# Kernel tuning notes

Measured on AMD Instinct MI355X. Metric: run time of the kernel, lower is better.

Reference implementation:

```python
import jax, jax.numpy as jnp
import numpy as np

N_NODES = 10000
N_EDGES = 640000
F_IN = 128
HID = 128
F_OUT = 40
BN_EPS = 1e-5


def setup_inputs() -> dict:
    key = jax.random.key(0)
    ks = jax.random.split(key, 8)
    x = jax.random.normal(ks[0], (N_NODES, F_IN), dtype=jnp.float32)
    edge_row = jax.random.randint(ks[1], (N_EDGES,), 0, N_NODES)
    edge_col = jax.random.randint(ks[2], (N_EDGES,), 0, N_NODES)
    edge_val = jax.random.uniform(ks[3], (N_EDGES,), dtype=jnp.float32)
    W1 = jax.random.normal(ks[4], (F_IN, HID), dtype=jnp.float32) * 0.05
    W2 = jax.random.normal(ks[5], (HID, HID), dtype=jnp.float32) * 0.05
    W3 = jax.random.normal(ks[6], (HID, F_OUT), dtype=jnp.float32) * 0.05
    return {
        "x": x, "edge_row": edge_row, "edge_col": edge_col, "edge_val": edge_val,
        "W1": W1, "b1": jnp.zeros((HID,), jnp.float32),
        "gamma2": jnp.ones((HID,), jnp.float32), "beta2": jnp.zeros((HID,), jnp.float32),
        "W2": W2, "b2": jnp.zeros((HID,), jnp.float32),
        "gamma3": jnp.ones((HID,), jnp.float32), "beta3": jnp.zeros((HID,), jnp.float32),
        "W3": W3, "b3": jnp.zeros((F_OUT,), jnp.float32),
    }


def _spmm(edge_row, edge_col, edge_val, x, n_nodes):
    # out[i] = sum_{e: row[e]==i} val[e] * x[col[e]]  == torch.sparse.mm(adj, x)
    msgs = edge_val[:, None] * jnp.take(x, edge_col, axis=0)  # [E, F]
    return jax.ops.segment_sum(msgs, edge_row, num_segments=n_nodes)


def _batchnorm(x, gamma, beta):
    # BatchNorm1d (training-mode normalization, biased variance)
    mean = jnp.mean(x, axis=0)
    var = jnp.mean(jnp.square(x - mean), axis=0)
    return gamma * (x - mean) * jax.lax.rsqrt(var + BN_EPS) + beta


def reference(x, edge_row, edge_col, edge_val, W1, b1, gamma2, beta2,
              W2, b2, gamma3, beta3, W3, b3):
    n = x.shape[0]
    # layer 1: SpMM -> Linear -> ReLU -> (dropout=identity in eval) -> BN
    h = _spmm(edge_row, edge_col, edge_val, x, n)
    h = jax.nn.relu(h @ W1 + b1)
    h = _batchnorm(h, gamma2, beta2)
    # layer 2
    h = _spmm(edge_row, edge_col, edge_val, h, n)
    h = jax.nn.relu(h @ W2 + b2)
    h = _batchnorm(h, gamma3, beta3)
    # layer 3
    h = _spmm(edge_row, edge_col, edge_val, h, n)
    h = h @ W3 + b3
    return jax.nn.log_softmax(h, axis=1)
```

## Files before the change

kernel.cpp:

```cpp
#include <hip/hip_runtime.h>
#include <hip/hip_bf16.h>
#include <math.h>

#define N_NODES 10000
#define F 128
#define F_OUT_ 40
#define N_EDGES_ 640000
#define BN_EPS 1e-5f
#define NBIN 625
#define RPB 16
#define NWGA 256
#define EPW 2500
#define BINCAP 1536
#define NREP 8

__device__ __forceinline__ unsigned pack4(int col, float v) {
    __hip_bfloat16 b = __float2bfloat16(v);
    return ((unsigned)(*(unsigned short*)&b) << 16) | (unsigned)col;
}
__device__ __forceinline__ int   col_of(unsigned q) { return (int)(q & 0xFFFFu); }
__device__ __forceinline__ float val_of(unsigned q) { return __uint_as_float(q & 0xFFFF0000u); }
__device__ __forceinline__ float lo16f(unsigned w) { return __uint_as_float(w << 16); }
__device__ __forceinline__ float hi16f(unsigned w) { return __uint_as_float(w & 0xffff0000u); }

__global__ __launch_bounds__(256) void fused_g1h(const float* __restrict__ x,
        const float* __restrict__ W1, __hip_bfloat16* __restrict__ T,
        const int* __restrict__ erow, int* __restrict__ hist,
        float* __restrict__ accsZ ) {
    __shared__ float Ws[F * F];
    __shared__ float As[16][F];
    __shared__ int   lh[NBIN];
    int tid = threadIdx.x;
    if (blockIdx.x == 0) {
        for (int i = tid; i < 2 * NREP * 256; i += 256) accsZ[i] = 0.f;
    }
    if (blockIdx.x >= NBIN) {
        int w = blockIdx.x - NBIN;
        for (int t = tid; t < NBIN; t += 256) lh[t] = 0;
        __syncthreads();
        int e0 = w * EPW;
        for (int e = e0 + tid; e < e0 + EPW; e += 256)
            atomicAdd(&lh[erow[e] >> 4], 1);
        __syncthreads();
        for (int t = tid; t < NBIN; t += 256) hist[w * NBIN + t] = lh[t];
        return;
    }
    for (int i = tid; i < F * F; i += 256) Ws[i] = W1[i];
    int r0 = blockIdx.x * 16;
    for (int i = tid; i < 16 * F; i += 256) {
        int r2 = i >> 7, k = i & (F - 1);
        As[r2][k] = x[(size_t)(r0 + r2) * F + k];
    }
    __syncthreads();
    int c = tid & (F - 1), hh = tid >> 7;
    for (int r2 = hh; r2 < 16; r2 += 2) {
        float acc = 0.f;
        #pragma unroll
        for (int k = 0; k < F; ++k) acc = fmaf(As[r2][k], Ws[k * F + c], acc);
        T[(size_t)(r0 + r2) * F + c] = __float2bfloat16(acc);
    }
}

__global__ __launch_bounds__(1024) void scatter_bin(const int* __restrict__ erow,
                                                    const int* __restrict__ ecol,
                                                    const float* __restrict__ eval_,
                                                    const int* __restrict__ hist,
                                                    int* __restrict__ base_g,
                                                    int2* __restrict__ ebin) {
    __shared__ int myoff[NBIN];
    __shared__ int tot[NBIN];
    __shared__ int cur[NBIN];
    __shared__ int sc[1024];
    int w = blockIdx.x, tid = threadIdx.x;
    for (int b = tid; b < NBIN; b += 1024) {
        int own = 0, all = 0;
        #pragma unroll 8
        for (int w2 = 0; w2 < NWGA; ++w2) {
            int h = hist[w2 * NBIN + b];
            all += h;
            if (w2 < w) own += h;
        }
        myoff[b] = own;
        tot[b] = all;
        cur[b] = 0;
    }
    __syncthreads();
    int val = (tid < NBIN) ? tot[tid] : 0;
    sc[tid] = val;
    __syncthreads();
    for (int off = 1; off < 1024; off <<= 1) {
        int v = 0;
        if (tid >= off) v = sc[tid - off];
        __syncthreads();
        if (tid >= off) sc[tid] += v;
        __syncthreads();
    }
    if (tid < NBIN) {
        int base = sc[tid] - val;
        myoff[tid] += base;
        if (w == 0) base_g[tid] = base;
    }
    if (w == 0 && tid == 0) base_g[NBIN] = N_EDGES_;
    __syncthreads();
    int e0 = w * EPW, e1 = e0 + EPW;
    for (int e = e0 + tid; e < e1; e += 1024) {
        int r = erow[e];
        int b = r >> 4;
        int p = atomicAdd(&cur[b], 1);
        ebin[myoff[b] + p] = make_int2((r << 14) | ecol[e], __float_as_int(eval_[e]));
    }
}

__global__ __launch_bounds__(256) void sort_bin(const int* __restrict__ base,
                                                const int2* __restrict__ ebin,
                                                unsigned* __restrict__ ebin2,
                                                int* __restrict__ rowptr) {
    __shared__ int2    ein[BINCAP];
    __shared__ unsigned eout[BINCAP];
    __shared__ int cnt16[16], pos16[16], exc[16];
    int b = blockIdx.x, tid = threadIdx.x;
    int lo = base[b], hi = base[b + 1];
    int n = min(hi - lo, BINCAP);
    for (int i = tid; i < n; i += 256) ein[i] = ebin[lo + i];
    if (tid < 16) cnt16[tid] = 0;
    __syncthreads();
    for (int i = tid; i < n; i += 256)
        atomicAdd(&cnt16[(ein[i].x >> 14) & 15], 1);
    __syncthreads();
    if (tid == 0) {
        int run = 0;
        #pragma unroll
        for (int j = 0; j < 16; ++j) { exc[j] = run; run += cnt16[j]; }
    }
    __syncthreads();
    if (tid < 16) {
        pos16[tid] = exc[tid];
        rowptr[b * RPB + tid] = lo + exc[tid];
    }
    if (b == NBIN - 1 && tid == 0) rowptr[N_NODES] = hi;
    __syncthreads();
    for (int i = tid; i < n; i += 256) {
        int2 q = ein[i];
        int j = (q.x >> 14) & 15;
        int p = atomicAdd(&pos16[j], 1);
        eout[p] = pack4(q.x & 16383, __int_as_float(q.y));
    }
    __syncthreads();
    for (int i = tid; i < n; i += 256) ebin2[lo + i] = eout[i];
}

__global__ __launch_bounds__(256) void spmm_row4s(const int* __restrict__ rowptr,
                                                  const unsigned* __restrict__ epk,
                                                  const unsigned long long* __restrict__ T8,
                                                  float* __restrict__ Z,
                                                  const float* __restrict__ bias,
                                                  float* __restrict__ accs) {
    __shared__ float sacc[2][F];
    int tid = threadIdx.x;
    for (int i = tid; i < 2 * F; i += 256) ((float*)sacc)[i] = 0.f;
    __syncthreads();
    int wv = tid >> 6, lane = tid & 63;
    int r = blockIdx.x * 4 + wv;
    int beg = rowptr[r], end = rowptr[r + 1];
    int half = lane >> 5, l2 = lane & 31;
    float a0c0 = 0.f, a0c1 = 0.f, a1c0 = 0.f, a1c1 = 0.f;
    float a2c0 = 0.f, a2c1 = 0.f, a3c0 = 0.f, a3c1 = 0.f;
    for (int bb = beg; bb < end; bb += 64) {
        int m = min(end - bb, 64);
        unsigned myq = (lane < m) ? epk[bb + lane] : 0u;
        int j = 0;
        for (; j + 16 <= m; j += 16) {
            unsigned q[8]; unsigned long long w[8];
            #pragma unroll
            for (int t = 0; t < 8; ++t) {
                q[t] = __shfl(myq, j + 2 * t + half);
                w[t] = __builtin_nontemporal_load(T8 + (unsigned)col_of(q[t]) * 32u + l2);
            }
            #pragma unroll
            for (int t = 0; t < 8; ++t) {
                float v = val_of(q[t]);
                unsigned wx = (unsigned)w[t], wy = (unsigned)(w[t] >> 32);
                if (t & 1) {
                    a0c1 = fmaf(v, lo16f(wx), a0c1);
                    a1c1 = fmaf(v, hi16f(wx), a1c1);
                    a2c1 = fmaf(v, lo16f(wy), a2c1);
                    a3c1 = fmaf(v, hi16f(wy), a3c1);
                } else {
                    a0c0 = fmaf(v, lo16f(wx), a0c0);
                    a1c0 = fmaf(v, hi16f(wx), a1c0);
                    a2c0 = fmaf(v, lo16f(wy), a2c0);
                    a3c0 = fmaf(v, hi16f(wy), a3c0);
                }
            }
        }
        for (; j + 2 <= m; j += 2) {
            unsigned q = __shfl(myq, j + half);
            unsigned long long w = __builtin_nontemporal_load(T8 + (unsigned)col_of(q) * 32u + l2);
            float v = val_of(q);
            unsigned wx = (unsigned)w, wy = (unsigned)(w >> 32);
            a0c0 = fmaf(v, lo16f(wx), a0c0);
            a1c0 = fmaf(v, hi16f(wx), a1c0);
            a2c0 = fmaf(v, lo16f(wy), a2c0);
            a3c0 = fmaf(v, hi16f(wy), a3c0);
        }
        if (j < m) {
            unsigned q = __shfl(myq, j);
            unsigned long long w = __builtin_nontemporal_load(T8 + (unsigned)col_of(q) * 32u + l2);
            float v = half ? 0.f : val_of(q);
            unsigned wx = (unsigned)w, wy = (unsigned)(w >> 32);
            a0c0 = fmaf(v, lo16f(wx), a0c0);
            a1c0 = fmaf(v, hi16f(wx), a1c0);
            a2c0 = fmaf(v, lo16f(wy), a2c0);
            a3c0 = fmaf(v, hi16f(wy), a3c0);
        }
    }
    float a0 = a0c0 + a0c1, a1 = a1c0 + a1c1;
    float a2 = a2c0 + a2c1, a3 = a3c0 + a3c1;
    a0 += __shfl_xor(a0, 32);
    a1 += __shfl_xor(a1, 32);
    a2 += __shfl_xor(a2, 32);
    a3 += __shfl_xor(a3, 32);
    if (half == 0) {
        *(float4*)(Z + (size_t)r * F + 4 * l2) = make_float4(a0, a1, a2, a3);
        float4 bi = *(const float4*)(bias + 4 * l2);
        float t0 = fmaxf(a0 + bi.x, 0.f), t1 = fmaxf(a1 + bi.y, 0.f);
        float t2 = fmaxf(a2 + bi.z, 0.f), t3 = fmaxf(a3 + bi.w, 0.f);
        atomicAdd(&sacc[0][4 * l2],     t0); atomicAdd(&sacc[1][4 * l2],     t0 * t0);
        atomicAdd(&sacc[0][4 * l2 + 1], t1); atomicAdd(&sacc[1][4 * l2 + 1], t1 * t1);
        atomicAdd(&sacc[0][4 * l2 + 2], t2); atomicAdd(&sacc[1][4 * l2 + 2], t2 * t2);
        atomicAdd(&sacc[0][4 * l2 + 3], t3); atomicAdd(&sacc[1][4 * l2 + 3], t3 * t3);
    }
    __syncthreads();
    int rep = blockIdx.x & (NREP - 1);
    float* dst = accs + rep * 2 * F;
    for (int i = tid; i < F; i += 256) {
        atomicAdd(&dst[i],     sacc[0][i]);
        atomicAdd(&dst[F + i], sacc[1][i]);
    }
}

__global__ __launch_bounds__(256) void spmm40_ls(const int* __restrict__ rowptr,
                                                 const unsigned* __restrict__ epk,
                                                 const unsigned short* __restrict__ T40,
                                                 const float* __restrict__ b3,
                                                 float* __restrict__ out) {
    int wv = threadIdx.x >> 6, lane = threadIdx.x & 63;
    int w = blockIdx.x * 4 + wv;
    if (w >= N_NODES) return;
    int beg = rowptr[w], end = rowptr[w + 1];
    float a[4] = {0.f, 0.f, 0.f, 0.f};
    const unsigned short* Tb = T40 + lane;
    bool act = (lane < F_OUT_);
    for (int base = beg; base < end; base += 64) {
        int m = min(end - base, 64);
        unsigned myq = 0;
        if (lane < m) myq = epk[base + lane];
        int j = 0;
        for (; j + 8 <= m; j += 8) {
            unsigned q[8];
            #pragma unroll
            for (int t = 0; t < 8; ++t) q[t] = __shfl(myq, j + t);
            if (act) {
                unsigned short u[8];
                #pragma unroll
                for (int t = 0; t < 8; ++t)
                    u[t] = __builtin_nontemporal_load(Tb + (unsigned)col_of(q[t]) * 40u);
                #pragma unroll
                for (int t = 0; t < 8; ++t)
                    a[t & 3] = fmaf(val_of(q[t]),
                                    __uint_as_float(((unsigned)u[t]) << 16), a[t & 3]);
            }
        }
        for (; j < m; ++j) {
            unsigned q = __shfl(myq, j);
            if (act) {
                unsigned short u = __builtin_nontemporal_load(Tb + (unsigned)col_of(q) * 40u);
                a[0] = fmaf(val_of(q), __uint_as_float(((unsigned)u) << 16), a[0]);
            }
        }
    }
    float acc = (a[0] + a[1]) + (a[2] + a[3]);
    float val = act ? acc + b3[lane] : -INFINITY;
    float m2 = val;
    #pragma unroll
    for (int off = 32; off > 0; off >>= 1) m2 = fmaxf(m2, __shfl_xor(m2, off));
    float e = act ? expf(val - m2) : 0.f;
    float s = e;
    #pragma unroll
    for (int off = 32; off > 0; off >>= 1) s += __shfl_xor(s, off);
    if (act) out[(size_t)w * F_OUT_ + lane] = val - m2 - logf(s);
}


__global__ __launch_bounds__(256) void gemm128_bn(const float* __restrict__ A,
        const float* __restrict__ W, const float* __restrict__ bias,
        const float* __restrict__ gamma, const float* __restrict__ beta,
        const float* __restrict__ accs, __hip_bfloat16* __restrict__ C) {
    __shared__ float Ws[F * F];
    __shared__ float As[16][F];
    __shared__ float sc[F], sh[F], bi[F];
    int tid = threadIdx.x;
    if (tid < F) {
        float s = 0.f, s2 = 0.f;
        #pragma unroll
        for (int rp = 0; rp < NREP; ++rp) {
            s  += accs[rp * 2 * F + tid];
            s2 += accs[rp * 2 * F + F + tid];
        }
        float m   = s / (float)N_NODES;
        float var = s2 / (float)N_NODES - m * m;
        float rs  = rsqrtf(var + BN_EPS);
        float g   = gamma[tid] * rs;
        sc[tid] = g;
        sh[tid] = beta[tid] - g * m;
        bi[tid] = bias[tid];
    }
    for (int i = tid; i < F * F; i += 256) Ws[i] = W[i];
    __syncthreads();
    int r0 = blockIdx.x * 16;
    for (int i = tid; i < 16 * F; i += 256) {
        int r2 = i >> 7, k = i & (F - 1);
        float a = A[(size_t)(r0 + r2) * F + k];
        As[r2][k] = fmaxf(a + bi[k], 0.f) * sc[k] + sh[k];
    }
    __syncthreads();
    int c = tid & (F - 1), hh = tid >> 7;
    for (int r2 = hh; r2 < 16; r2 += 2) {
        float acc = 0.f;
        #pragma unroll
        for (int k = 0; k < F; ++k) acc = fmaf(As[r2][k], Ws[k * F + c], acc);
        C[(size_t)(r0 + r2) * F + c] = __float2bfloat16(acc);
    }
}

__global__ __launch_bounds__(256) void gemm40_bn(const float* __restrict__ A,
        const float* __restrict__ W, const float* __restrict__ bias,
        const float* __restrict__ gamma, const float* __restrict__ beta,
        const float* __restrict__ accs, __hip_bfloat16* __restrict__ C) {
    __shared__ float Ws[F * F_OUT_];
    __shared__ float sc[F], sh[F], bi[F];
    int tid = threadIdx.x;
    if (tid < F) {
        float s = 0.f, s2 = 0.f;
        #pragma unroll
        for (int rp = 0; rp < NREP; ++rp) {
            s  += accs[rp * 2 * F + tid];
            s2 += accs[rp * 2 * F + F + tid];
        }
        float m   = s / (float)N_NODES;
        float var = s2 / (float)N_NODES - m * m;
        float rs  = rsqrtf(var + BN_EPS);
        float g   = gamma[tid] * rs;
        sc[tid] = g;
        sh[tid] = beta[tid] - g * m;
        bi[tid] = bias[tid];
    }
    for (int i = tid; i < F * F_OUT_; i += 256) Ws[i] = W[i];
    __syncthreads();
    int c = tid % F_OUT_, rl = tid / F_OUT_;
    if (rl >= 6) return;
    int r = blockIdx.x * 6 + rl;
    if (r >= N_NODES) return;
    const float* a = A + (size_t)r * F;
    float acc = 0.f;
    #pragma unroll
    for (int k = 0; k < F; ++k) {
        float t = fmaxf(a[k] + bi[k], 0.f) * sc[k] + sh[k];
        acc = fmaf(t, Ws[k * F_OUT_ + c], acc);
    }
    C[(size_t)r * F_OUT_ + c] = __float2bfloat16(acc);
}


extern "C" void kernel_launch(void* const* d_in, const int* in_sizes, int n_in,
                              void* d_out, int out_size, void* d_ws, size_t ws_size,
                              hipStream_t stream) {
    const float* x      = (const float*)d_in[0];
    const int*   erow   = (const int*)  d_in[1];
    const int*   ecol   = (const int*)  d_in[2];
    const float* eval_  = (const float*)d_in[3];
    const float* W1     = (const float*)d_in[4];
    const float* b1     = (const float*)d_in[5];
    const float* gamma2 = (const float*)d_in[6];
    const float* beta2  = (const float*)d_in[7];
    const float* W2     = (const float*)d_in[8];
    const float* b2     = (const float*)d_in[9];
    const float* gamma3 = (const float*)d_in[10];
    const float* beta3  = (const float*)d_in[11];
    const float* W3     = (const float*)d_in[12];
    const float* b3     = (const float*)d_in[13];
    float* out = (float*)d_out;

    const size_t nf = (size_t)N_NODES * F;
    const int BLK = 256;

    int*   hist   = (int*)d_ws;
    int*   base_g = hist + NWGA * NBIN;
    float* accsA  = (float*)(base_g + 626);
    float* accsB  = accsA + NREP * 256;
    int*   rowptr = (int*)(accsB + NREP * 256);
    __hip_bfloat16* T = (__hip_bfloat16*)(rowptr + 10016);
    float* Z     = (float*)((char*)T + nf * 2);
    int2*  ebin  = (int2*)(Z + nf);
    unsigned* ebin2 = (unsigned*)(ebin + N_EDGES_);

    fused_g1h<<<NBIN + NWGA, BLK, 0, stream>>>(x, W1, T, erow, hist, accsA);
    scatter_bin<<<NWGA, 1024, 0, stream>>>(erow, ecol, eval_, hist, base_g, ebin);
    sort_bin<<<NBIN, BLK, 0, stream>>>(base_g, ebin, ebin2, rowptr);

    const int GB4 = N_NODES / 4;

    spmm_row4s<<<GB4, BLK, 0, stream>>>(rowptr, ebin2, (const unsigned long long*)T, Z, b1, accsA);

    gemm128_bn<<<NBIN, BLK, 0, stream>>>(Z, W2, b1, gamma2, beta2, accsA, T);
    spmm_row4s<<<GB4, BLK, 0, stream>>>(rowptr, ebin2, (const unsigned long long*)T, Z, b2, accsB);

    gemm40_bn<<<(N_NODES + 5) / 6, BLK, 0, stream>>>(Z, W3, b2, gamma3, beta3, accsB, T);
    spmm40_ls<<<GB4, BLK, 0, stream>>>(rowptr, ebin2, (const unsigned short*)T, b3, out);
}
```

Baseline: 162.8 us.

## Halve binning workgroups, unroll scatter loop, and switch gather loads' cache policy

The edge-binning kernel now runs half as many workgroups, each handling twice as many edges. Its scatter loop is unrolled four-way so that independent row, column and value loads and shared-memory atomics are in flight together. In the SpMM kernels, the nontemporal gathers of bf16 feature rows are replaced by relaxed agent-scope atomic loads (128-wide layer) and plain loads (40-wide layer), so reused rows can stay cached. Fewer binning workgroups lowers parallelism, and the atomic-load path may change instruction codegen or cache behaviour in ways that are hard to predict.

New measurement: 144.0 us. 1.13x faster.

```diff
diff --git a/kernel.cpp b/kernel.cpp
--- a/kernel.cpp
+++ b/kernel.cpp
@@ -9,8 +9,8 @@
 #define BN_EPS 1e-5f
 #define NBIN 625
 #define RPB 16
-#define NWGA 256
-#define EPW 2500
+#define NWGA 128
+#define EPW 5000
 #define BINCAP 1536
 #define NREP 8
 
@@ -22,6 +22,10 @@
 __device__ __forceinline__ float val_of(unsigned q) { return __uint_as_float(q & 0xFFFF0000u); }
 __device__ __forceinline__ float lo16f(unsigned w) { return __uint_as_float(w << 16); }
 __device__ __forceinline__ float hi16f(unsigned w) { return __uint_as_float(w & 0xffff0000u); }
+
+__device__ __forceinline__ unsigned long long ldg_l2(const unsigned long long* p) {
+    return __hip_atomic_load(p, __ATOMIC_RELAXED, __HIP_MEMORY_SCOPE_AGENT);
+}
 
 __global__ __launch_bounds__(256) void fused_g1h(const float* __restrict__ x,
         const float* __restrict__ W1, __hip_bfloat16* __restrict__ T,
@@ -103,7 +107,22 @@
     if (w == 0 && tid == 0) base_g[NBIN] = N_EDGES_;
     __syncthreads();
     int e0 = w * EPW, e1 = e0 + EPW;
-    for (int e = e0 + tid; e < e1; e += 1024) {
+    int e = e0 + tid;
+    for (; e + 3072 < e1; e += 4096) {
+        int   r0 = erow[e],        r1 = erow[e + 1024],  r2 = erow[e + 2048],  r3 = erow[e + 3072];
+        int   c0 = ecol[e],        c1 = ecol[e + 1024],  c2 = ecol[e + 2048],  c3 = ecol[e + 3072];
+        float v0 = eval_[e],       v1 = eval_[e + 1024], v2 = eval_[e + 2048], v3 = eval_[e + 3072];
+        int b0 = r0 >> 4, b1 = r1 >> 4, b2 = r2 >> 4, b3 = r3 >> 4;
+        int p0 = atomicAdd(&cur[b0], 1);
+        int p1 = atomicAdd(&cur[b1], 1);
+        int p2 = atomicAdd(&cur[b2], 1);
+        int p3 = atomicAdd(&cur[b3], 1);
+        ebin[myoff[b0] + p0] = make_int2((r0 << 14) | c0, __float_as_int(v0));
+        ebin[myoff[b1] + p1] = make_int2((r1 << 14) | c1, __float_as_int(v1));
+        ebin[myoff[b2] + p2] = make_int2((r2 << 14) | c2, __float_as_int(v2));
+        ebin[myoff[b3] + p3] = make_int2((r3 << 14) | c3, __float_as_int(v3));
+    }
+    for (; e < e1; e += 1024) {
         int r = erow[e];
         int b = r >> 4;
         int p = atomicAdd(&cur[b], 1);
@@ -174,7 +193,7 @@
             #pragma unroll
             for (int t = 0; t < 8; ++t) {
                 q[t] = __shfl(myq, j + 2 * t + half);
-                w[t] = __builtin_nontemporal_load(T8 + (unsigned)col_of(q[t]) * 32u + l2);
+                w[t] = ldg_l2(T8 + (unsigned)col_of(q[t]) * 32u + l2);
             }
             #pragma unroll
             for (int t = 0; t < 8; ++t) {
@@ -195,7 +214,7 @@
         }
         for (; j + 2 <= m; j += 2) {
             unsigned q = __shfl(myq, j + half);
-            unsigned long long w = __builtin_nontemporal_load(T8 + (unsigned)col_of(q) * 32u + l2);
+            unsigned long long w = ldg_l2(T8 + (unsigned)col_of(q) * 32u + l2);
             float v = val_of(q);
             unsigned wx = (unsigned)w, wy = (unsigned)(w >> 32);
             a0c0 = fmaf(v, lo16f(wx), a0c0);
@@ -205,7 +224,7 @@
         }
         if (j < m) {
             unsigned q = __shfl(myq, j);
-            unsigned long long w = __builtin_nontemporal_load(T8 + (unsigned)col_of(q) * 32u + l2);
+            unsigned long long w = ldg_l2(T8 + (unsigned)col_of(q) * 32u + l2);
             float v = half ? 0.f : val_of(q);
             unsigned wx = (unsigned)w, wy = (unsigned)(w >> 32);
             a0c0 = fmaf(v, lo16f(wx), a0c0);
@@ -263,8 +282,7 @@
             if (act) {
                 unsigned short u[8];
                 #pragma unroll
-                for (int t = 0; t < 8; ++t)
-                    u[t] = __builtin_nontemporal_load(Tb + (unsigned)col_of(q[t]) * 40u);
+                for (int t = 0; t < 8; ++t) u[t] = Tb[(unsigned)col_of(q[t]) * 40u];
                 #pragma unroll
                 for (int t = 0; t < 8; ++t)
                     a[t & 3] = fmaf(val_of(q[t]),
@@ -274,7 +292,7 @@
         for (; j < m; ++j) {
             unsigned q = __shfl(myq, j);
             if (act) {
-                unsigned short u = __builtin_nontemporal_load(Tb + (unsigned)col_of(q) * 40u);
+                unsigned short u = Tb[(unsigned)col_of(q) * 40u];
                 a[0] = fmaf(val_of(q), __uint_as_float(((unsigned)u) << 16), a[0]);
             }
         }
```
